# Kernel optimization log

Hardware: AMD Instinct MI355X
Metric: run time of the kernel (lower is better)

The kernel has to match this reference:

```python
import jax, jax.numpy as jnp
import numpy as np

N_NODES = 50000
N_EDGES = 800000
N_GRAPHS = 512
HIDDEN = 256
NODE_FEAT = 9
LAYERS = 4


def setup_inputs() -> dict:
    key = jax.random.key(0)
    ks = jax.random.split(key, 9)
    x = jax.random.normal(ks[0], (N_NODES, NODE_FEAT), dtype=jnp.float32)
    edge_index = jax.random.randint(ks[1], (2, N_EDGES), 0, N_NODES, dtype=jnp.int64)
    batch = jnp.sort(jax.random.randint(ks[2], (N_NODES,), 0, N_GRAPHS, dtype=jnp.int64))
    embed_W = jax.random.normal(ks[3], (NODE_FEAT, HIDDEN), dtype=jnp.float32) * (1.0 / np.sqrt(NODE_FEAT))
    embed_b = jnp.zeros((HIDDEN,), dtype=jnp.float32)
    conv_W = jax.random.normal(ks[4], (LAYERS, HIDDEN, HIDDEN), dtype=jnp.float32) * (1.0 / np.sqrt(HIDDEN))
    conv_b = jnp.zeros((LAYERS, HIDDEN), dtype=jnp.float32)
    out_W = jax.random.normal(ks[5], (HIDDEN, 1), dtype=jnp.float32) * (1.0 / np.sqrt(HIDDEN))
    out_b = jnp.zeros((1,), dtype=jnp.float32)
    return {"x": x, "edge_index": edge_index, "batch": batch,
            "embed_W": embed_W, "embed_b": embed_b,
            "conv_W": conv_W, "conv_b": conv_b,
            "out_W": out_W, "out_b": out_b}


def reference(x, edge_index, batch, embed_W, embed_b, conv_W, conv_b, out_W, out_b):
    n = x.shape[0]
    src, dst = edge_index[0], edge_index[1]
    # GCN symmetric normalization with self-loops: deg includes the self-loop (+1)
    deg = jax.ops.segment_sum(jnp.ones(src.shape[0], x.dtype), dst, num_segments=n) + 1.0
    dinv = jax.lax.rsqrt(deg)                       # [N]
    norm_e = dinv[src] * dinv[dst]                  # [E] edge coefficient
    self_coef = (dinv * dinv)[:, None]              # [N,1] self-loop coefficient

    h = jax.nn.relu(x @ embed_W + embed_b)          # [N,H]
    for l in range(conv_W.shape[0]):
        hw = h @ conv_W[l]                          # [N,H] transform first
        msg = hw[src] * norm_e[:, None]             # [E,H] gather + scale
        agg = jax.ops.segment_sum(msg, dst, num_segments=n)  # scatter-add
        agg = agg + hw * self_coef                  # self-loop contribution
        h = jax.nn.relu(agg + conv_b[l])

    # global mean pool over graph ids
    sums = jax.ops.segment_sum(h, batch, num_segments=N_GRAPHS)           # [G,H]
    cnt = jax.ops.segment_sum(jnp.ones(n, h.dtype), batch, num_segments=N_GRAPHS)
    pooled = sums / jnp.maximum(cnt, 1.0)[:, None]
    return pooled @ out_W + out_b                   # [G,1]
```

## Files before the change

### kernel.cpp

```cpp
#include <hip/hip_runtime.h>

#define N_NODES 50000
#define N_EDGES 800000
#define N_GRAPHS 512
#define HIDDEN 256
#define NODE_FEAT 9
#define LAYERS 4
#define BUCKET 64

typedef float floatx4 __attribute__((ext_vector_type(4)));
typedef short short8 __attribute__((ext_vector_type(8)));
typedef unsigned uint2v __attribute__((ext_vector_type(2)));

__device__ __forceinline__ float bf2f(unsigned u) {
    unsigned v = u << 16;
    float f;
    __builtin_memcpy(&f, &v, 4);
    return f;
}
__device__ __forceinline__ unsigned short f2bf(float f) {
    unsigned v;
    __builtin_memcpy(&v, &f, 4);
    v += 0x7FFFu + ((v >> 16) & 1u);
    return (unsigned short)(v >> 16);
}

__global__ void fillb_kernel(const int* __restrict__ src, const int* __restrict__ dst,
                             int* __restrict__ cnt, int* __restrict__ col_src, int E) {
    int e = blockIdx.x * blockDim.x + threadIdx.x;
    if (e < E) {
        int d = dst[e];
        int pos = atomicAdd(&cnt[d], 1);
        if (pos < BUCKET) col_src[d * BUCKET + pos] = src[e];
    }
}

__global__ __launch_bounds__(256) void aux_kernel(const int* __restrict__ cnt,
                                                  float* __restrict__ dinv,
                                                  const int* __restrict__ batch,
                                                  int* __restrict__ gstart) {
    int i = blockIdx.x * 256 + threadIdx.x;
    if (i < N_NODES) dinv[i] = rsqrtf((float)(cnt[i] + 1));
    int g = i - N_NODES;
    if (g >= 0 && g <= N_GRAPHS) {
        if (g == N_GRAPHS) { gstart[g] = N_NODES; return; }
        int lo = 0, hi = N_NODES;
        while (lo < hi) {
            int mid = (lo + hi) >> 1;
            if (batch[mid] < g) lo = mid + 1; else hi = mid;
        }
        gstart[g] = lo;
    }
}

__global__ __launch_bounds__(256) void packW_kernel(const float* __restrict__ W,
                                                    unsigned short* __restrict__ Wsw) {
    int idx = blockIdx.x * 256 + threadIdx.x;
    int lane = idx & 63;
    int ct   = (idx >> 6) & 15;
    int ks   = (idx >> 10) & 7;
    int l    = idx >> 13;
    int n = ct * 16 + (lane & 15);
    int kbase = ks * 32 + (lane >> 4) * 8;
    const float* Wl = W + (size_t)l * HIDDEN * HIDDEN;
    alignas(16) unsigned short tmp[8];
    #pragma unroll
    for (int j = 0; j < 8; j++)
        tmp[j] = f2bf(Wl[(size_t)(kbase + j) * HIDDEN + n]);
    *(uint4*)&Wsw[(size_t)idx * 8] = *(const uint4*)tmp;
}

__global__ __launch_bounds__(256, 2) void embed_gemm(const float* __restrict__ x,
                                                     const float* __restrict__ embW,
                                                     const float* __restrict__ embb,
                                                     const unsigned short* __restrict__ Wsw,
                                                     unsigned short* __restrict__ hwout, int N) {
    __shared__ unsigned short As[64][264];
    int t = threadIdx.x;
    int wv = t >> 6, lane = t & 63, quad = lane >> 4, l15 = lane & 15;
    int n0 = blockIdx.x * 64;

    const short8* Wl = (const short8*)Wsw;
    short8 bq[3][4];
    #pragma unroll
    for (int p = 0; p < 2; p++)
        #pragma unroll
        for (int ci = 0; ci < 4; ci++)
            bq[p][ci] = Wl[(size_t)(p * 16 + wv * 4 + ci) * 64 + lane];

    #pragma unroll 2
    for (int i = 0; i < 8; i++) {
        int j = t + i * 256;
        int r = j >> 5;
        int c8 = j & 31;
        int n = n0 + r;
        unsigned o0 = 0, o1 = 0, o2 = 0, o3 = 0;
        if (n < N) {
            float xr[NODE_FEAT];
            #pragma unroll
            for (int k = 0; k < NODE_FEAT; k++) xr[k] = x[(size_t)n * NODE_FEAT + k];
            float4 a0 = *(const float4*)&embb[c8 * 8];
            float4 a1 = *(const float4*)&embb[c8 * 8 + 4];
            #pragma unroll
            for (int k = 0; k < NODE_FEAT; k++) {
                float4 w0 = *(const float4*)&embW[k * HIDDEN + c8 * 8];
                float4 w1 = *(const float4*)&embW[k * HIDDEN + c8 * 8 + 4];
                a0.x += xr[k] * w0.x; a0.y += xr[k] * w0.y;
                a0.z += xr[k] * w0.z; a0.w += xr[k] * w0.w;
                a1.x += xr[k] * w1.x; a1.y += xr[k] * w1.y;
                a1.z += xr[k] * w1.z; a1.w += xr[k] * w1.w;
            }
            o0 = (unsigned)f2bf(fmaxf(a0.x, 0.f)) | ((unsigned)f2bf(fmaxf(a0.y, 0.f)) << 16);
            o1 = (unsigned)f2bf(fmaxf(a0.z, 0.f)) | ((unsigned)f2bf(fmaxf(a0.w, 0.f)) << 16);
            o2 = (unsigned)f2bf(fmaxf(a1.x, 0.f)) | ((unsigned)f2bf(fmaxf(a1.y, 0.f)) << 16);
            o3 = (unsigned)f2bf(fmaxf(a1.z, 0.f)) | ((unsigned)f2bf(fmaxf(a1.w, 0.f)) << 16);
        }
        *(uint4*)&As[r][c8 * 8] = make_uint4(o0, o1, o2, o3);
    }
    __syncthreads();

    floatx4 acc[4][4];
    #pragma unroll
    for (int i = 0; i < 4; i++)
        #pragma unroll
        for (int j = 0; j < 4; j++)
            acc[i][j] = (floatx4){0.f, 0.f, 0.f, 0.f};

    #pragma unroll
    for (int ks = 0; ks < 8; ks++) {
        if (ks < 6) {
            #pragma unroll
            for (int ci = 0; ci < 4; ci++)
                bq[(ks + 2) % 3][ci] = Wl[(size_t)((ks + 2) * 16 + wv * 4 + ci) * 64 + lane];
        }
        short8 a[4];
        #pragma unroll
        for (int rt = 0; rt < 4; rt++)
            a[rt] = *(const short8*)&As[rt * 16 + l15][ks * 32 + quad * 8];
        #pragma unroll
        for (int rt = 0; rt < 4; rt++)
            #pragma unroll
            for (int ci = 0; ci < 4; ci++)
                acc[rt][ci] = __builtin_amdgcn_mfma_f32_16x16x32_bf16(a[rt], bq[ks % 3][ci], acc[rt][ci], 0, 0, 0);
    }

    __syncthreads();
    #pragma unroll
    for (int rt = 0; rt < 4; rt++) {
        #pragma unroll
        for (int ci = 0; ci < 4; ci++) {
            int col = (wv * 4 + ci) * 16 + l15;
            int rowb = rt * 16 + quad * 4;
            #pragma unroll
            for (int reg = 0; reg < 4; reg++)
                As[rowb + reg][col] = f2bf(acc[rt][ci][reg]);
        }
    }
    __syncthreads();
    #pragma unroll
    for (int i = 0; i < 8; i++) {
        int j = t + i * 256;
        int r = j >> 5;
        int c = j & 31;
        int n = n0 + r;
        if (n < N)
            *(uint4*)&hwout[(size_t)n * HIDDEN + c * 8] = *(const uint4*)&As[r][c * 8];
    }
}

__global__ __launch_bounds__(256, 2) void gemm_mfma(const unsigned short* __restrict__ hin,
                                                    const unsigned short* __restrict__ Wsw,
                                                    unsigned short* __restrict__ hwout, int N) {
    __shared__ unsigned short As[64][264];
    int t = threadIdx.x;
    int wv = t >> 6, lane = t & 63, quad = lane >> 4, l15 = lane & 15;
    int n0 = blockIdx.x * 64;
    const uint4* h4 = (const uint4*)hin;

    uint4 av[8];
    #pragma unroll
    for (int i = 0; i < 8; i++) {
        int j = t + i * 256;
        int r = j >> 5;
        int c = j & 31;
        int n = n0 + r;
        av[i] = make_uint4(0u, 0u, 0u, 0u);
        if (n < N) av[i] = h4[(size_t)n * 32 + c];
    }
    const short8* Wl = (const short8*)Wsw;
    short8 bq[3][4];
    #pragma unroll
    for (int p = 0; p < 2; p++)
        #pragma unroll
        for (int ci = 0; ci < 4; ci++)
            bq[p][ci] = Wl[(size_t)(p * 16 + wv * 4 + ci) * 64 + lane];
    #pragma unroll
    for (int i = 0; i < 8; i++) {
        int j = t + i * 256;
        int r = j >> 5;
        int c = j & 31;
        *(uint4*)&As[r][c * 8] = av[i];
    }
    __syncthreads();

    floatx4 acc[4][4];
    #pragma unroll
    for (int i = 0; i < 4; i++)
        #pragma unroll
        for (int j = 0; j < 4; j++)
            acc[i][j] = (floatx4){0.f, 0.f, 0.f, 0.f};

    #pragma unroll
    for (int ks = 0; ks < 8; ks++) {
        if (ks < 6) {
            #pragma unroll
            for (int ci = 0; ci < 4; ci++)
                bq[(ks + 2) % 3][ci] = Wl[(size_t)((ks + 2) * 16 + wv * 4 + ci) * 64 + lane];
        }
        short8 a[4];
        #pragma unroll
        for (int rt = 0; rt < 4; rt++)
            a[rt] = *(const short8*)&As[rt * 16 + l15][ks * 32 + quad * 8];
        #pragma unroll
        for (int rt = 0; rt < 4; rt++)
            #pragma unroll
            for (int ci = 0; ci < 4; ci++)
                acc[rt][ci] = __builtin_amdgcn_mfma_f32_16x16x32_bf16(a[rt], bq[ks % 3][ci], acc[rt][ci], 0, 0, 0);
    }

    __syncthreads();
    #pragma unroll
    for (int rt = 0; rt < 4; rt++) {
        #pragma unroll
        for (int ci = 0; ci < 4; ci++) {
            int col = (wv * 4 + ci) * 16 + l15;
            int rowb = rt * 16 + quad * 4;
            #pragma unroll
            for (int reg = 0; reg < 4; reg++)
                As[rowb + reg][col] = f2bf(acc[rt][ci][reg]);
        }
    }
    __syncthreads();
    #pragma unroll
    for (int i = 0; i < 8; i++) {
        int j = t + i * 256;
        int r = j >> 5;
        int c = j & 31;
        int n = n0 + r;
        if (n < N)
            *(uint4*)&hwout[(size_t)n * HIDDEN + c * 8] = *(const uint4*)&As[r][c * 8];
    }
}

__global__ __launch_bounds__(256) void agg_kernel(const unsigned short* __restrict__ hw,
                                                  const int* __restrict__ cnt,
                                                  const int* __restrict__ col_src,
                                                  const float* __restrict__ dinv,
                                                  const float* __restrict__ bias,
                                                  unsigned short* __restrict__ hout) {
    __shared__ uint2 sEdge[4][64];
    int wv = threadIdx.x >> 6, lane = threadIdx.x & 63;
    int n = blockIdx.x * 4 + wv;
    if (n >= N_NODES) return;
    float dn = dinv[n];
    int deg = cnt[n]; if (deg > BUCKET) deg = BUCKET;

    uint2 s2 = ((const uint2*)(hw + (size_t)n * HIDDEN))[lane];
    float4 b4 = *(const float4*)&bias[4 * lane];
    float selfc = dn * dn;
    float a0 = bf2f(s2.x & 0xFFFFu) * selfc + b4.x;
    float a1 = bf2f(s2.x >> 16)     * selfc + b4.y;
    float a2 = bf2f(s2.y & 0xFFFFu) * selfc + b4.z;
    float a3 = bf2f(s2.y >> 16)     * selfc + b4.w;

    if (lane < deg) {
        int s = col_src[n * BUCKET + lane];
        float nr = dinv[s] * dn;
        unsigned nrb;
        __builtin_memcpy(&nrb, &nr, 4);
        sEdge[wv][lane] = make_uint2((unsigned)s, nrb);
    }
    for (int i = 0; i < deg; i++) {
        uint2 p = sEdge[wv][i];
        float nr;
        __builtin_memcpy(&nr, &p.y, 4);
        uint2 u = ((const uint2*)(hw + (size_t)p.x * HIDDEN))[lane];
        a0 += nr * bf2f(u.x & 0xFFFFu);
        a1 += nr * bf2f(u.x >> 16);
        a2 += nr * bf2f(u.y & 0xFFFFu);
        a3 += nr * bf2f(u.y >> 16);
    }
    unsigned p0 = (unsigned)f2bf(fmaxf(a0, 0.0f)) | ((unsigned)f2bf(fmaxf(a1, 0.0f)) << 16);
    unsigned p1 = (unsigned)f2bf(fmaxf(a2, 0.0f)) | ((unsigned)f2bf(fmaxf(a3, 0.0f)) << 16);
    uint2v pv; pv.x = p0; pv.y = p1;
    __builtin_nontemporal_store(pv, (uint2v*)(hout + (size_t)n * HIDDEN) + lane);
}

__global__ __launch_bounds__(256) void agg_dot_kernel(const unsigned short* __restrict__ hw,
                                                      const int* __restrict__ cnt,
                                                      const int* __restrict__ col_src,
                                                      const float* __restrict__ dinv,
                                                      const float* __restrict__ bias,
                                                      const float* __restrict__ outW,
                                                      float* __restrict__ dotv) {
    __shared__ uint2 sEdge[4][64];
    int wv = threadIdx.x >> 6, lane = threadIdx.x & 63;
    int n = blockIdx.x * 4 + wv;
    if (n >= N_NODES) return;
    float dn = dinv[n];
    int deg = cnt[n]; if (deg > BUCKET) deg = BUCKET;

    uint2 s2 = ((const uint2*)(hw + (size_t)n * HIDDEN))[lane];
    float4 b4 = *(const float4*)&bias[4 * lane];
    float selfc = dn * dn;
    float a0 = bf2f(s2.x & 0xFFFFu) * selfc + b4.x;
    float a1 = bf2f(s2.x >> 16)     * selfc + b4.y;
    float a2 = bf2f(s2.y & 0xFFFFu) * selfc + b4.z;
    float a3 = bf2f(s2.y >> 16)     * selfc + b4.w;

    if (lane < deg) {
        int s = col_src[n * BUCKET + lane];
        float nr = dinv[s] * dn;
        unsigned nrb;
        __builtin_memcpy(&nrb, &nr, 4);
        sEdge[wv][lane] = make_uint2((unsigned)s, nrb);
    }
    for (int i = 0; i < deg; i++) {
        uint2 p = sEdge[wv][i];
        float nr;
        __builtin_memcpy(&nr, &p.y, 4);
        uint2 u = ((const uint2*)(hw + (size_t)p.x * HIDDEN))[lane];
        a0 += nr * bf2f(u.x & 0xFFFFu);
        a1 += nr * bf2f(u.x >> 16);
        a2 += nr * bf2f(u.y & 0xFFFFu);
        a3 += nr * bf2f(u.y >> 16);
    }
    float4 w = *(const float4*)&outW[4 * lane];
    float dot = fmaxf(a0, 0.0f) * w.x + fmaxf(a1, 0.0f) * w.y
              + fmaxf(a2, 0.0f) * w.z + fmaxf(a3, 0.0f) * w.w;
    #pragma unroll
    for (int off = 32; off > 0; off >>= 1) dot += __shfl_xor(dot, off, 64);
    if (lane == 0) dotv[n] = dot;
}

__global__ __launch_bounds__(64) void finalize_kernel(const float* __restrict__ dotv,
                                                      const int* __restrict__ gstart,
                                                      const float* __restrict__ outb,
                                                      float* __restrict__ out) {
    int g = blockIdx.x;
    int lane = threadIdx.x;
    int s = gstart[g], e = gstart[g + 1];
    float acc = 0.0f;
    for (int n = s + lane; n < e; n += 64) acc += dotv[n];
    #pragma unroll
    for (int off = 32; off > 0; off >>= 1) acc += __shfl_xor(acc, off, 64);
    if (lane == 0) out[g] = acc / fmaxf((float)(e - s), 1.0f) + outb[0];
}

extern "C" void kernel_launch(void* const* d_in, const int* in_sizes, int n_in,
                              void* d_out, int out_size, void* d_ws, size_t ws_size,
                              hipStream_t stream) {
    const float* x     = (const float*)d_in[0];
    const int*   edge  = (const int*)d_in[1];
    const int*   src   = edge;
    const int*   dst   = edge + N_EDGES;
    const int*   batch = (const int*)d_in[2];
    const float* embW  = (const float*)d_in[3];
    const float* embb  = (const float*)d_in[4];
    const float* convW = (const float*)d_in[5];
    const float* convb = (const float*)d_in[6];
    const float* outW  = (const float*)d_in[7];
    const float* outb  = (const float*)d_in[8];
    float* out = (float*)d_out;

    char* ws = (char*)d_ws;
    size_t off = 0;
    auto take = [&](size_t bytes) { char* p = ws + off; off += (bytes + 255) & ~(size_t)255; return p; };
    int*   cnt     = (int*)  take((size_t)N_NODES * 4);
    int*   col_src = (int*)  take((size_t)N_NODES * BUCKET * 4);
    float* dinv    = (float*)take((size_t)N_NODES * 4);
    int*   gstart  = (int*)  take((size_t)(N_GRAPHS + 1) * 4);
    float* dotv    = (float*)take((size_t)N_NODES * 4);
    unsigned short* Wsw = (unsigned short*)take((size_t)LAYERS * 8 * 16 * 64 * 8 * 2);
    unsigned short* h0  = (unsigned short*)take((size_t)N_NODES * HIDDEN * 2);
    unsigned short* h1  = (unsigned short*)take((size_t)N_NODES * HIDDEN * 2);

    hipMemsetAsync(cnt, 0, (size_t)N_NODES * 4, stream);

    fillb_kernel<<<(N_EDGES + 255) / 256, 256, 0, stream>>>(src, dst, cnt, col_src, N_EDGES);
    aux_kernel<<<(N_NODES + N_GRAPHS + 1 + 255) / 256, 256, 0, stream>>>(cnt, dinv, batch, gstart);
    packW_kernel<<<128, 256, 0, stream>>>(convW, Wsw);

    int nblk = (N_NODES + 63) / 64;
    int ablk = (N_NODES + 3) / 4;

    embed_gemm<<<nblk, 256, 0, stream>>>(x, embW, embb, Wsw, h1, N_NODES);
    agg_kernel<<<ablk, 256, 0, stream>>>(h1, cnt, col_src, dinv, convb + 0 * HIDDEN, h0);
    gemm_mfma<<<nblk, 256, 0, stream>>>(h0, Wsw + (size_t)1 * 65536, h1, N_NODES);
    agg_kernel<<<ablk, 256, 0, stream>>>(h1, cnt, col_src, dinv, convb + 1 * HIDDEN, h0);
    gemm_mfma<<<nblk, 256, 0, stream>>>(h0, Wsw + (size_t)2 * 65536, h1, N_NODES);
    agg_kernel<<<ablk, 256, 0, stream>>>(h1, cnt, col_src, dinv, convb + 2 * HIDDEN, h0);
    gemm_mfma<<<nblk, 256, 0, stream>>>(h0, Wsw + (size_t)3 * 65536, h1, N_NODES);
    agg_dot_kernel<<<ablk, 256, 0, stream>>>(h1, cnt, col_src, dinv, convb + 3 * HIDDEN, outW, dotv);

    finalize_kernel<<<N_GRAPHS, 64, 0, stream>>>(dotv, gstart, outb, out);
}
```

Measured before the change: 438.8 us.

## Fuse edge bucketing into embed GEMM and enlarge GEMM row tile to 128

The edge-bucketing pass is folded into the embedding GEMM launch: 3125 blocks run, the first 782 also compute the embedding GEMM, and every block scatters 256 edges into the CSR buckets. This removes one kernel launch and lets the atomic scatter overlap with GEMM work. Separately, the conv GEMM tile grows from 64 to 128 rows per block, halving the grid and reusing each weight fragment across twice as many rows, at the cost of more accumulator registers and twice the shared memory per block, which may reduce occupancy.

```diff
diff --git a/kernel.cpp b/kernel.cpp
--- a/kernel.cpp
+++ b/kernel.cpp
@@ -7,6 +7,9 @@
 #define NODE_FEAT 9
 #define LAYERS 4
 #define BUCKET 64
+#define NGEMM1 782
+#define NT128 391
+#define EBLK 3125
 
 typedef float floatx4 __attribute__((ext_vector_type(4)));
 typedef short short8 __attribute__((ext_vector_type(8)));
@@ -23,16 +26,6 @@
     __builtin_memcpy(&v, &f, 4);
     v += 0x7FFFu + ((v >> 16) & 1u);
     return (unsigned short)(v >> 16);
-}
-
-__global__ void fillb_kernel(const int* __restrict__ src, const int* __restrict__ dst,
-                             int* __restrict__ cnt, int* __restrict__ col_src, int E) {
-    int e = blockIdx.x * blockDim.x + threadIdx.x;
-    if (e < E) {
-        int d = dst[e];
-        int pos = atomicAdd(&cnt[d], 1);
-        if (pos < BUCKET) col_src[d * BUCKET + pos] = src[e];
-    }
 }
 
 __global__ __launch_bounds__(256) void aux_kernel(const int* __restrict__ cnt,
@@ -74,54 +67,161 @@
                                                      const float* __restrict__ embW,
                                                      const float* __restrict__ embb,
                                                      const unsigned short* __restrict__ Wsw,
-                                                     unsigned short* __restrict__ hwout, int N) {
+                                                     unsigned short* __restrict__ hwout, int N,
+                                                     const int* __restrict__ srcE,
+                                                     const int* __restrict__ dstE,
+                                                     int* __restrict__ cnt,
+                                                     int* __restrict__ col_src) {
     __shared__ unsigned short As[64][264];
     int t = threadIdx.x;
+    if (blockIdx.x < NGEMM1) {
+        int wv = t >> 6, lane = t & 63, quad = lane >> 4, l15 = lane & 15;
+        int n0 = blockIdx.x * 64;
+
+        const short8* Wl = (const short8*)Wsw;
+        short8 bq[3][4];
+        #pragma unroll
+        for (int p = 0; p < 2; p++)
+            #pragma unroll
+            for (int ci = 0; ci < 4; ci++)
+                bq[p][ci] = Wl[(size_t)(p * 16 + wv * 4 + ci) * 64 + lane];
+
+        #pragma unroll 2
+        for (int i = 0; i < 8; i++) {
+            int j = t + i * 256;
+            int r = j >> 5;
+            int c8 = j & 31;
+            int n = n0 + r;
+            unsigned o0 = 0, o1 = 0, o2 = 0, o3 = 0;
+            if (n < N) {
+                float xr[NODE_FEAT];
+                #pragma unroll
+                for (int k = 0; k < NODE_FEAT; k++) xr[k] = x[(size_t)n * NODE_FEAT + k];
+                float4 a0 = *(const float4*)&embb[c8 * 8];
+                float4 a1 = *(const float4*)&embb[c8 * 8 + 4];
+                #pragma unroll
+                for (int k = 0; k < NODE_FEAT; k++) {
+                    float4 w0 = *(const float4*)&embW[k * HIDDEN + c8 * 8];
+                    float4 w1 = *(const float4*)&embW[k * HIDDEN + c8 * 8 + 4];
+                    a0.x += xr[k] * w0.x; a0.y += xr[k] * w0.y;
+                    a0.z += xr[k] * w0.z; a0.w += xr[k] * w0.w;
+                    a1.x += xr[k] * w1.x; a1.y += xr[k] * w1.y;
+                    a1.z += xr[k] * w1.z; a1.w += xr[k] * w1.w;
+                }
+                o0 = (unsigned)f2bf(fmaxf(a0.x, 0.f)) | ((unsigned)f2bf(fmaxf(a0.y, 0.f)) << 16);
+                o1 = (unsigned)f2bf(fmaxf(a0.z, 0.f)) | ((unsigned)f2bf(fmaxf(a0.w, 0.f)) << 16);
+                o2 = (unsigned)f2bf(fmaxf(a1.x, 0.f)) | ((unsigned)f2bf(fmaxf(a1.y, 0.f)) << 16);
+                o3 = (unsigned)f2bf(fmaxf(a1.z, 0.f)) | ((unsigned)f2bf(fmaxf(a1.w, 0.f)) << 16);
+            }
+            *(uint4*)&As[r][c8 * 8] = make_uint4(o0, o1, o2, o3);
+        }
+        __syncthreads();
+
+        floatx4 acc[4][4];
+        #pragma unroll
+        for (int i = 0; i < 4; i++)
+            #pragma unroll
+            for (int j = 0; j < 4; j++)
+                acc[i][j] = (floatx4){0.f, 0.f, 0.f, 0.f};
+
+        #pragma unroll
+        for (int ks = 0; ks < 8; ks++) {
+            if (ks < 6) {
+                #pragma unroll
+                for (int ci = 0; ci < 4; ci++)
+                    bq[(ks + 2) % 3][ci] = Wl[(size_t)((ks + 2) * 16 + wv * 4 + ci) * 64 + lane];
+            }
+            short8 a[4];
+            #pragma unroll
+            for (int rt = 0; rt < 4; rt++)
+                a[rt] = *(const short8*)&As[rt * 16 + l15][ks * 32 + quad * 8];
+            #pragma unroll
+            for (int rt = 0; rt < 4; rt++)
+                #pragma unroll
+                for (int ci = 0; ci < 4; ci++)
+                    acc[rt][ci] = __builtin_amdgcn_mfma_f32_16x16x32_bf16(a[rt], bq[ks % 3][ci], acc[rt][ci], 0, 0, 0);
+        }
+
+        __syncthreads();
+        #pragma unroll
+        for (int rt = 0; rt < 4; rt++) {
+            #pragma unroll
+            for (int ci = 0; ci < 4; ci++) {
+                int col = (wv * 4 + ci) * 16 + l15;
+                int rowb = rt * 16 + quad * 4;
+                #pragma unroll
+                for (int reg = 0; reg < 4; reg++)
+                    As[rowb + reg][col] = f2bf(acc[rt][ci][reg]);
+            }
+        }
+        __syncthreads();
+        #pragma unroll
+        for (int i = 0; i < 8; i++) {
+            int j = t + i * 256;
+            int r = j >> 5;
+            int c = j & 31;
+            int n = n0 + r;
+            if (n < N)
+                *(uint4*)&hwout[(size_t)n * HIDDEN + c * 8] = *(const uint4*)&As[r][c * 8];
+        }
+    }
+
+    int e = blockIdx.x * 256 + t;
+    int d = dstE[e];
+    int pos = atomicAdd(&cnt[d], 1);
+    if (pos < BUCKET) col_src[d * BUCKET + pos] = srcE[e];
+}
+
+__global__ __launch_bounds__(256, 2) void gemm_mfma(const unsigned short* __restrict__ hin,
+                                                    const unsigned short* __restrict__ Wsw,
+                                                    unsigned short* __restrict__ hwout, int N) {
+    __shared__ unsigned short As[128][264];
+    int t = threadIdx.x;
     int wv = t >> 6, lane = t & 63, quad = lane >> 4, l15 = lane & 15;
-    int n0 = blockIdx.x * 64;
-
+    int n0 = blockIdx.x * 128;
+    const uint4* h4 = (const uint4*)hin;
     const short8* Wl = (const short8*)Wsw;
+
+    uint4 av[8];
+    #pragma unroll
+    for (int i = 0; i < 8; i++) {
+        int j = t + i * 256;
+        int r = j >> 5, c = j & 31;
+        int n = n0 + r;
+        av[i] = make_uint4(0u, 0u, 0u, 0u);
+        if (n < N) av[i] = h4[(size_t)n * 32 + c];
+    }
     short8 bq[3][4];
     #pragma unroll
     for (int p = 0; p < 2; p++)
         #pragma unroll
         for (int ci = 0; ci < 4; ci++)
             bq[p][ci] = Wl[(size_t)(p * 16 + wv * 4 + ci) * 64 + lane];
-
-    #pragma unroll 2
+    #pragma unroll
     for (int i = 0; i < 8; i++) {
         int j = t + i * 256;
-        int r = j >> 5;
-        int c8 = j & 31;
+        int r = j >> 5, c = j & 31;
+        *(uint4*)&As[r][c * 8] = av[i];
+    }
+    #pragma unroll
+    for (int i = 0; i < 8; i++) {
+        int j = t + (i + 8) * 256;
+        int r = j >> 5, c = j & 31;
         int n = n0 + r;
-        unsigned o0 = 0, o1 = 0, o2 = 0, o3 = 0;
-        if (n < N) {
-            float xr[NODE_FEAT];
-            #pragma unroll
-            for (int k = 0; k < NODE_FEAT; k++) xr[k] = x[(size_t)n * NODE_FEAT + k];
-            float4 a0 = *(const float4*)&embb[c8 * 8];
-            float4 a1 = *(const float4*)&embb[c8 * 8 + 4];
-            #pragma unroll
-            for (int k = 0; k < NODE_FEAT; k++) {
-                float4 w0 = *(const float4*)&embW[k * HIDDEN + c8 * 8];
-                float4 w1 = *(const float4*)&embW[k * HIDDEN + c8 * 8 + 4];
-                a0.x += xr[k] * w0.x; a0.y += xr[k] * w0.y;
-                a0.z += xr[k] * w0.z; a0.w += xr[k] * w0.w;
-                a1.x += xr[k] * w1.x; a1.y += xr[k] * w1.y;
-                a1.z += xr[k] * w1.z; a1.w += xr[k] * w1.w;
-            }
-            o0 = (unsigned)f2bf(fmaxf(a0.x, 0.f)) | ((unsigned)f2bf(fmaxf(a0.y, 0.f)) << 16);
-            o1 = (unsigned)f2bf(fmaxf(a0.z, 0.f)) | ((unsigned)f2bf(fmaxf(a0.w, 0.f)) << 16);
-            o2 = (unsigned)f2bf(fmaxf(a1.x, 0.f)) | ((unsigned)f2bf(fmaxf(a1.y, 0.f)) << 16);
-            o3 = (unsigned)f2bf(fmaxf(a1.z, 0.f)) | ((unsigned)f2bf(fmaxf(a1.w, 0.f)) << 16);
-        }
-        *(uint4*)&As[r][c8 * 8] = make_uint4(o0, o1, o2, o3);
+        av[i] = make_uint4(0u, 0u, 0u, 0u);
+        if (n < N) av[i] = h4[(size_t)n * 32 + c];
+    }
+    #pragma unroll
+    for (int i = 0; i < 8; i++) {
+        int j = t + (i + 8) * 256;
+        int r = j >> 5, c = j & 31;
+        *(uint4*)&As[r][c * 8] = av[i];
     }
     __syncthreads();
 
-    floatx4 acc[4][4];
-    #pragma unroll
-    for (int i = 0; i < 4; i++)
+    floatx4 acc[8][4];
+    #pragma unroll
+    for (int i = 0; i < 8; i++)
         #pragma unroll
         for (int j = 0; j < 4; j++)
             acc[i][j] = (floatx4){0.f, 0.f, 0.f, 0.f};
@@ -133,20 +233,18 @@
             for (int ci = 0; ci < 4; ci++)
                 bq[(ks + 2) % 3][ci] = Wl[(size_t)((ks + 2) * 16 + wv * 4 + ci) * 64 + lane];
         }
-        short8 a[4];
-        #pragma unroll
-        for (int rt = 0; rt < 4; rt++)
-            a[rt] = *(const short8*)&As[rt * 16 + l15][ks * 32 + quad * 8];
-        #pragma unroll
-        for (int rt = 0; rt < 4; rt++)
+        #pragma unroll
+        for (int rt = 0; rt < 8; rt++) {
+            short8 a = *(const short8*)&As[rt * 16 + l15][ks * 32 + quad * 8];
             #pragma unroll
             for (int ci = 0; ci < 4; ci++)
-                acc[rt][ci] = __builtin_amdgcn_mfma_f32_16x16x32_bf16(a[rt], bq[ks % 3][ci], acc[rt][ci], 0, 0, 0);
+                acc[rt][ci] = __builtin_amdgcn_mfma_f32_16x16x32_bf16(a, bq[ks % 3][ci], acc[rt][ci], 0, 0, 0);
+        }
     }
 
     __syncthreads();
     #pragma unroll
-    for (int rt = 0; rt < 4; rt++) {
+    for (int rt = 0; rt < 8; rt++) {
         #pragma unroll
         for (int ci = 0; ci < 4; ci++) {
             int col = (wv * 4 + ci) * 16 + l15;
@@ -158,94 +256,9 @@
     }
     __syncthreads();
     #pragma unroll
-    for (int i = 0; i < 8; i++) {
+    for (int i = 0; i < 16; i++) {
         int j = t + i * 256;
-        int r = j >> 5;
-        int c = j & 31;
-        int n = n0 + r;
-        if (n < N)
-            *(uint4*)&hwout[(size_t)n * HIDDEN + c * 8] = *(const uint4*)&As[r][c * 8];
-    }
-}
-
-__global__ __launch_bounds__(256, 2) void gemm_mfma(const unsigned short* __restrict__ hin,
-                                                    const unsigned short* __restrict__ Wsw,
-                                                    unsigned short* __restrict__ hwout, int N) {
-    __shared__ unsigned short As[64][264];
-    int t = threadIdx.x;
-    int wv = t >> 6, lane = t & 63, quad = lane >> 4, l15 = lane & 15;
-    int n0 = blockIdx.x * 64;
-    const uint4* h4 = (const uint4*)hin;
-
-    uint4 av[8];
-    #pragma unroll
-    for (int i = 0; i < 8; i++) {
-        int j = t + i * 256;
-        int r = j >> 5;
-        int c = j & 31;
-        int n = n0 + r;
-        av[i] = make_uint4(0u, 0u, 0u, 0u);
-        if (n < N) av[i] = h4[(size_t)n * 32 + c];
-    }
-    const short8* Wl = (const short8*)Wsw;
-    short8 bq[3][4];
-    #pragma unroll
-    for (int p = 0; p < 2; p++)
-        #pragma unroll
-        for (int ci = 0; ci < 4; ci++)
-            bq[p][ci] = Wl[(size_t)(p * 16 + wv * 4 + ci) * 64 + lane];
-    #pragma unroll
-    for (int i = 0; i < 8; i++) {
-        int j = t + i * 256;
-        int r = j >> 5;
-        int c = j & 31;
-        *(uint4*)&As[r][c * 8] = av[i];
-    }
-    __syncthreads();
-
-    floatx4 acc[4][4];
-    #pragma unroll
-    for (int i = 0; i < 4; i++)
-        #pragma unroll
-        for (int j = 0; j < 4; j++)
-            acc[i][j] = (floatx4){0.f, 0.f, 0.f, 0.f};
-
-    #pragma unroll
-    for (int ks = 0; ks < 8; ks++) {
-        if (ks < 6) {
-            #pragma unroll
-            for (int ci = 0; ci < 4; ci++)
-                bq[(ks + 2) % 3][ci] = Wl[(size_t)((ks + 2) * 16 + wv * 4 + ci) * 64 + lane];
-        }
-        short8 a[4];
-        #pragma unroll
-        for (int rt = 0; rt < 4; rt++)
-            a[rt] = *(const short8*)&As[rt * 16 + l15][ks * 32 + quad * 8];
-        #pragma unroll
-        for (int rt = 0; rt < 4; rt++)
-            #pragma unroll
-            for (int ci = 0; ci < 4; ci++)
-                acc[rt][ci] = __builtin_amdgcn_mfma_f32_16x16x32_bf16(a[rt], bq[ks % 3][ci], acc[rt][ci], 0, 0, 0);
-    }
-
-    __syncthreads();
-    #pragma unroll
-    for (int rt = 0; rt < 4; rt++) {
-        #pragma unroll
-        for (int ci = 0; ci < 4; ci++) {
-            int col = (wv * 4 + ci) * 16 + l15;
-            int rowb = rt * 16 + quad * 4;
-            #pragma unroll
-            for (int reg = 0; reg < 4; reg++)
-                As[rowb + reg][col] = f2bf(acc[rt][ci][reg]);
-        }
-    }
-    __syncthreads();
-    #pragma unroll
-    for (int i = 0; i < 8; i++) {
-        int j = t + i * 256;
-        int r = j >> 5;
-        int c = j & 31;
+        int r = j >> 5, c = j & 31;
         int n = n0 + r;
         if (n < N)
             *(uint4*)&hwout[(size_t)n * HIDDEN + c * 8] = *(const uint4*)&As[r][c * 8];
@@ -387,20 +400,19 @@
 
     hipMemsetAsync(cnt, 0, (size_t)N_NODES * 4, stream);
 
-    fillb_kernel<<<(N_EDGES + 255) / 256, 256, 0, stream>>>(src, dst, cnt, col_src, N_EDGES);
+    packW_kernel<<<128, 256, 0, stream>>>(convW, Wsw);
+
+    int ablk = (N_NODES + 3) / 4;
+
+    embed_gemm<<<EBLK, 256, 0, stream>>>(x, embW, embb, Wsw, h1, N_NODES,
+                                         src, dst, cnt, col_src);
     aux_kernel<<<(N_NODES + N_GRAPHS + 1 + 255) / 256, 256, 0, stream>>>(cnt, dinv, batch, gstart);
-    packW_kernel<<<128, 256, 0, stream>>>(convW, Wsw);
-
-    int nblk = (N_NODES + 63) / 64;
-    int ablk = (N_NODES + 3) / 4;
-
-    embed_gemm<<<nblk, 256, 0, stream>>>(x, embW, embb, Wsw, h1, N_NODES);
     agg_kernel<<<ablk, 256, 0, stream>>>(h1, cnt, col_src, dinv, convb + 0 * HIDDEN, h0);
-    gemm_mfma<<<nblk, 256, 0, stream>>>(h0, Wsw + (size_t)1 * 65536, h1, N_NODES);
+    gemm_mfma<<<NT128, 256, 0, stream>>>(h0, Wsw + (size_t)1 * 65536, h1, N_NODES);
     agg_kernel<<<ablk, 256, 0, stream>>>(h1, cnt, col_src, dinv, convb + 1 * HIDDEN, h0);
-    gemm_mfma<<<nblk, 256, 0, stream>>>(h0, Wsw + (size_t)2 * 65536, h1, N_NODES);
+    gemm_mfma<<<NT128, 256, 0, stream>>>(h0, Wsw + (size_t)2 * 65536, h1, N_NODES);
     agg_kernel<<<ablk, 256, 0, stream>>>(h1, cnt, col_src, dinv, convb + 2 * HIDDEN, h0);
-    gemm_mfma<<<nblk, 256, 0, stream>>>(h0, Wsw + (size_t)3 * 65536, h1, N_NODES);
+    gemm_mfma<<<NT128, 256, 0, stream>>>(h0, Wsw + (size_t)3 * 65536, h1, N_NODES);
     agg_dot_kernel<<<ablk, 256, 0, stream>>>(h1, cnt, col_src, dinv, convb + 3 * HIDDEN, outW, dotv);
 
     finalize_kernel<<<N_GRAPHS, 64, 0, stream>>>(dotv, gstart, outb, out);
```

New measurement: 451.6 us. 2.9% more time.
